# Kernel tuning notes

Measured on AMD Instinct MI355X. Metric: run time of the kernel, lower is better.

## Reference

```python
import jax, jax.numpy as jnp
import numpy as np

NUM_ENT = 40000
NUM_REL = 20


def _rgcn_layer(x, src, dst, et, comp, basis, root, bias, act):
    # Basis decomposition: W_r = sum_b comp[r, b] * basis[b]  -> [R, in, out]
    W = jnp.einsum('rb,bio->rio', comp, basis)
    # Per-(dst, relation) sum of source features: equivalent to per-edge
    # transform W_{et[e]} @ x[src[e]] then scatter-sum, but transforms after
    # aggregation (linear, so identical math) to avoid an [E, in, out] gather.
    seg = dst * NUM_REL + et                       # combined segment id
    S = jax.ops.segment_sum(x[src], seg, num_segments=NUM_ENT * NUM_REL)
    S = S.reshape(NUM_ENT, NUM_REL, x.shape[1])    # [N, R, in]
    agg = jnp.einsum('nri,rio->no', S, W)          # [N, out]
    # mean aggregation over ALL incoming edges (PyG RGCNConv aggr='mean')
    deg = jax.ops.segment_sum(jnp.ones(src.shape[0], x.dtype), dst,
                              num_segments=NUM_ENT)
    agg = agg / jnp.clip(deg, 1.0)[:, None]
    out = agg + x @ root + bias
    return jnp.tanh(out) if act else out


def setup_inputs() -> dict:
    key = jax.random.key(0)
    ks = jax.random.split(key, 16)
    E = 640000
    d = 128
    B = 8
    s = 0.05
    return {
        'edge_index': jax.random.randint(ks[0], (2, E), 0, NUM_ENT),
        'edge_type': jax.random.randint(ks[1], (E,), 0, NUM_REL),
        'init_embed': jax.random.normal(ks[2], (NUM_ENT, d), jnp.float32) * s,
        'init_rel': jax.random.normal(ks[3], (NUM_REL * 2, d), jnp.float32) * s,
        'w_rel': jax.random.normal(ks[4], (d, d), jnp.float32) * s,
        'comp1': jax.random.normal(ks[5], (NUM_REL, B), jnp.float32) * s,
        'basis1': jax.random.normal(ks[6], (B, d, d), jnp.float32) * s,
        'root1': jax.random.normal(ks[7], (d, d), jnp.float32) * s,
        'bias1': jax.random.normal(ks[8], (d,), jnp.float32) * s,
        'comp2': jax.random.normal(ks[9], (NUM_REL, B), jnp.float32) * s,
        'basis2': jax.random.normal(ks[10], (B, d, d), jnp.float32) * s,
        'root2': jax.random.normal(ks[11], (d, d), jnp.float32) * s,
        'bias2': jax.random.normal(ks[12], (d,), jnp.float32) * s,
    }


def reference(edge_index, edge_type, init_embed, init_rel, w_rel,
              comp1, basis1, root1, bias1, comp2, basis2, root2, bias2):
    src, dst = edge_index[0], edge_index[1]
    x = init_embed
    # layer 1: init_dim -> gcn_dim, act=tanh (gcn_layer=2)
    x = _rgcn_layer(x, src, dst, edge_type, comp1, basis1, root1, bias1, True)
    # dropout is identity at inference
    # layer 2: embed_dim -> embed_dim, act=None
    x = _rgcn_layer(x, src, dst, edge_type, comp2, basis2, root2, bias2, False)
    r = init_rel @ w_rel
    return (x, r)
```

## Files before the change

### kernel.cpp

```cpp
#include <hip/hip_runtime.h>
#include <hip/hip_bf16.h>

#define NENT 40000
#define NREL 20
#define DIM 128
#define NBASIS 8
#define TILE 32
#define PKCAP 1024
#define SCANBLK 157

typedef __attribute__((ext_vector_type(8))) short sh8;
typedef __attribute__((ext_vector_type(4))) float fx4;

__device__ __forceinline__ short f2bf(float f) {
    union { __hip_bfloat16 h; short s; } u;
    u.h = __float2bfloat16(f);
    return u.s;
}

__global__ void k_tobf(const float* __restrict__ x, ushort* __restrict__ xb, int nelem) {
    int i = (blockIdx.x * 256 + threadIdx.x) * 4;
    if (i >= nelem) return;
    float4 v = *(const float4*)(x + i);
    ushort4 o;
    o.x = (ushort)f2bf(v.x); o.y = (ushort)f2bf(v.y);
    o.z = (ushort)f2bf(v.z); o.w = (ushort)f2bf(v.w);
    *(ushort4*)(xb + i) = o;
}

__global__ void k_wfrag9(const float* __restrict__ basis, const float* __restrict__ root,
                         short* __restrict__ Wfb) {
    int t = blockIdx.x * 256 + threadIdx.x;
    if (t >= 9 * 16384) return;
    int ks = t / 16384;
    int rem = t & 16383;
    int i = rem >> 7, o = rem & 127;
    float v = (ks < 8) ? basis[ks * 16384 + i * 128 + o] : root[i * 128 + o];
    int c = o >> 4, l15 = o & 15;
    int kk = i >> 5, lhi = (i >> 3) & 3, e = i & 7;
    int lane = l15 + lhi * 16;
    Wfb[(size_t)ks * 16384 + (size_t)(((c * 4 + kk) * 64 + lane) << 3) + e] = f2bf(v);
}

__global__ void k_hist(const int* __restrict__ dst, int E, int* __restrict__ hist) {
    int e = blockIdx.x * 256 + threadIdx.x;
    if (e < E) atomicAdd(&hist[dst[e]], 1);
}

__global__ void k_scan1(const int* __restrict__ hist, int* __restrict__ offs,
                        int* __restrict__ bsum) {
    __shared__ int ps[256];
    int t = threadIdx.x;
    int i = blockIdx.x * 256 + t;
    int v = (i < NENT) ? hist[i] : 0;
    ps[t] = v;
    __syncthreads();
    for (int off = 1; off < 256; off <<= 1) {
        int u = (t >= off) ? ps[t - off] : 0;
        __syncthreads();
        ps[t] += u;
        __syncthreads();
    }
    if (i < NENT) offs[i] = ps[t] - v;
    if (t == 255) bsum[blockIdx.x] = ps[255];
}

__global__ void k_scan2(int* __restrict__ bsum) {
    __shared__ int ps[256];
    int t = threadIdx.x;
    int v = (t < SCANBLK) ? bsum[t] : 0;
    ps[t] = v;
    __syncthreads();
    for (int off = 1; off < 256; off <<= 1) {
        int u = (t >= off) ? ps[t - off] : 0;
        __syncthreads();
        ps[t] += u;
        __syncthreads();
    }
    if (t < SCANBLK) bsum[t] = ps[t] - v;
}

__global__ void k_scan3(int* __restrict__ offs, int* __restrict__ cursor,
                        const int* __restrict__ bsum, int E) {
    int i = blockIdx.x * 256 + threadIdx.x;
    if (i < NENT) {
        int o = offs[i] + bsum[blockIdx.x];
        offs[i] = o;
        cursor[i] = o;
    }
    if (i == 0) offs[NENT] = E;
}

__global__ void k_scatter(const int* __restrict__ et, const int* __restrict__ srcA,
                          const int* __restrict__ dstA, int E,
                          int* __restrict__ cursor, unsigned* __restrict__ packed) {
    int e = blockIdx.x * 256 + threadIdx.x;
    if (e >= E) return;
    int pos = atomicAdd(&cursor[dstA[e]], 1);
    packed[pos] = (unsigned)srcA[e] | ((unsigned)et[e] << 16);
}

#define GLDD(dst, ptr)                                                     \
    asm volatile("global_load_dword %0, %1, off" : "=v"(dst) : "v"(ptr))

#define WAITV(N)                                                           \
    do {                                                                   \
        asm volatile("s_waitcnt vmcnt(" #N ")" ::: "memory");              \
        __builtin_amdgcn_sched_barrier(0);                                 \
    } while (0)

__global__ __launch_bounds__(512) void k_fused(
    const ushort* __restrict__ xb, const unsigned* __restrict__ packed,
    const int* __restrict__ offs, const float* __restrict__ comp,
    const short* __restrict__ Wfb, const float* __restrict__ bias,
    ushort* __restrict__ outbf, float* __restrict__ outf, int act) {
    __shared__ __align__(16) ushort Gl[TILE * 1024];
    __shared__ __align__(16) float cl[NREL * NBASIS];
    __shared__ __align__(16) unsigned pkl[PKCAP];

    int t = threadIdx.x;
    int lane = t & 63, wid = t >> 6;
    if (t < NREL * NBASIS) cl[t] = comp[t];

    int tile0 = blockIdx.x * TILE;
    int base = offs[tile0];
    int totE = offs[tile0 + TILE] - base;
    for (int i = t; i < totE && i < PKCAP; i += 512) pkl[i] = packed[base + i];
    __syncthreads();

    const unsigned* xrow = (const unsigned*)xb + lane;
    bool fast = (totE <= PKCAP);
    for (int sub = 0; sub < 4; ++sub) {
        int row = wid * 4 + sub;
        int n = tile0 + row;
        int begg = offs[n];
        int cnt = offs[n + 1] - begg;
        int begl = begg - base;

        float a0[NBASIS], a1[NBASIS];
#pragma unroll
        for (int b = 0; b < NBASIS; ++b) { a0[b] = 0.f; a1[b] = 0.f; }

        if (cnt > 0 && fast) {
            unsigned p0v = pkl[begl];
            unsigned pA[8], pB[8], rA[8], rB[8];

            auto ldp = [&](int i0, unsigned (&p)[8]) {
#pragma unroll
                for (int u = 0; u < 8; ++u) {
                    int i = i0 + u;
                    p[u] = (i < cnt) ? pkl[begl + i] : p0v;
                }
            };
            auto issue = [&](const unsigned (&p)[8], unsigned (&r)[8]) {
#pragma unroll
                for (int u = 0; u < 8; ++u) {
                    const unsigned* ap = xrow + (size_t)(p[u] & 0xFFFFu) * 64;
                    GLDD(r[u], ap);
                }
            };
            auto proc = [&](int i0, const unsigned (&p)[8], const unsigned (&r)[8]) {
#pragma unroll
                for (int u = 0; u < 8; ++u) {
                    if (i0 + u < cnt) {
                        float xlo = __uint_as_float(r[u] << 16);
                        float xhi = __uint_as_float(r[u] & 0xFFFF0000u);
                        int et = p[u] >> 16;
                        float4 cwa = *(const float4*)&cl[et * NBASIS];
                        float4 cwb = *(const float4*)&cl[et * NBASIS + 4];
                        a0[0] += cwa.x * xlo; a1[0] += cwa.x * xhi;
                        a0[1] += cwa.y * xlo; a1[1] += cwa.y * xhi;
                        a0[2] += cwa.z * xlo; a1[2] += cwa.z * xhi;
                        a0[3] += cwa.w * xlo; a1[3] += cwa.w * xhi;
                        a0[4] += cwb.x * xlo; a1[4] += cwb.x * xhi;
                        a0[5] += cwb.y * xlo; a1[5] += cwb.y * xhi;
                        a0[6] += cwb.z * xlo; a1[6] += cwb.z * xhi;
                        a0[7] += cwb.w * xlo; a1[7] += cwb.w * xhi;
                    }
                }
            };

            ldp(0, pA); issue(pA, rA);
            int i0 = 0;
            while (i0 < cnt) {
                ldp(i0 + 8, pB); issue(pB, rB);
                WAITV(8);
                proc(i0, pA, rA);
                i0 += 8;
                if (i0 >= cnt) break;
                ldp(i0 + 8, pA); issue(pA, rA);
                WAITV(8);
                proc(i0, pB, rB);
                i0 += 8;
            }
            asm volatile("s_waitcnt vmcnt(0)" ::: "memory");
            __builtin_amdgcn_sched_barrier(0);
        } else if (cnt > 0) {
            unsigned pA = packed[begg], pB = 0, rA = xrow[(size_t)(pA & 0xFFFFu) * 64];
            if (cnt > 1) pB = packed[begg + 1];
            for (int i = 0; i < cnt; ++i) {
                unsigned pC = (i + 2 < cnt) ? packed[begg + i + 2] : 0u;
                unsigned rB = xrow[(size_t)(pB & 0xFFFFu) * 64];
                float xlo = __uint_as_float(rA << 16);
                float xhi = __uint_as_float(rA & 0xFFFF0000u);
                int et = pA >> 16;
                float4 cwa = *(const float4*)&cl[et * NBASIS];
                float4 cwb = *(const float4*)&cl[et * NBASIS + 4];
                a0[0] += cwa.x * xlo; a1[0] += cwa.x * xhi;
                a0[1] += cwa.y * xlo; a1[1] += cwa.y * xhi;
                a0[2] += cwa.z * xlo; a1[2] += cwa.z * xhi;
                a0[3] += cwa.w * xlo; a1[3] += cwa.w * xhi;
                a0[4] += cwb.x * xlo; a1[4] += cwb.x * xhi;
                a0[5] += cwb.y * xlo; a1[5] += cwb.y * xhi;
                a0[6] += cwb.z * xlo; a1[6] += cwb.z * xhi;
                a0[7] += cwb.w * xlo; a1[7] += cwb.w * xhi;
                pA = pB; pB = pC; rA = rB;
            }
        }

        float inv = 1.f / (float)(cnt < 1 ? 1 : cnt);
#pragma unroll
        for (int b = 0; b < NBASIS; ++b) {
            unsigned lo = (unsigned)(ushort)f2bf(a0[b] * inv);
            unsigned hi = (unsigned)(ushort)f2bf(a1[b] * inv);
            unsigned byteoff = (unsigned)(row * 2048 + b * 256 + lane * 4);
            byteoff ^= (unsigned)((row & 7) << 4);
            *(unsigned*)((char*)Gl + byteoff) = lo | (hi << 16);
        }
    }
    __syncthreads();

    int wr = wid >> 2, wc = wid & 3;
    int l15 = lane & 15, lhi = lane >> 4;
    int arow = wr * 16 + l15;

    fx4 acc0 = (fx4){0.f, 0.f, 0.f, 0.f};
    fx4 acc1 = (fx4){0.f, 0.f, 0.f, 0.f};

    const ushort* Xr = xb + (size_t)(tile0 + wr * 16 + l15) * 128 + lhi * 8;
    const sh8* W8 = (const sh8*)Wfb;
    int c0 = wc * 2, c1 = wc * 2 + 1;

#pragma unroll
    for (int ks = 0; ks < 9; ++ks) {
        sh8 a[4];
        if (ks < 8) {
#pragma unroll
            for (int kk = 0; kk < 4; ++kk) {
                unsigned byteoff = (unsigned)(arow * 2048 + ks * 256 + kk * 64 + lhi * 16);
                byteoff ^= (unsigned)((arow & 7) << 4);
                a[kk] = *(const sh8*)((const char*)Gl + byteoff);
            }
        } else {
#pragma unroll
            for (int kk = 0; kk < 4; ++kk) a[kk] = *(const sh8*)(Xr + kk * 32);
        }
#pragma unroll
        for (int kk = 0; kk < 4; ++kk) {
            sh8 b0 = W8[(size_t)ks * 2048 + (size_t)((c0 * 4 + kk) * 64 + lane)];
            sh8 b1 = W8[(size_t)ks * 2048 + (size_t)((c1 * 4 + kk) * 64 + lane)];
            acc0 = __builtin_amdgcn_mfma_f32_16x16x32_bf16(a[kk], b0, acc0, 0, 0, 0);
            acc1 = __builtin_amdgcn_mfma_f32_16x16x32_bf16(a[kk], b1, acc1, 0, 0, 0);
        }
    }

    int orow0 = tile0 + wr * 16 + lhi * 4;
#pragma unroll
    for (int cc = 0; cc < 2; ++cc) {
        int col = wc * 32 + cc * 16 + l15;
        float bv = bias[col];
        const fx4& ac = cc ? acc1 : acc0;
#pragma unroll
        for (int j = 0; j < 4; ++j) {
            float v = ac[j] + bv;
            if (act) {
                v = tanhf(v);
                outbf[(size_t)(orow0 + j) * 128 + col] = (ushort)f2bf(v);
            } else {
                outf[(size_t)(orow0 + j) * 128 + col] = v;
            }
        }
    }
}

__global__ void k_rel(const float* __restrict__ rel, const float* __restrict__ wrel,
                      float* __restrict__ out, int nrows) {
    int idx = blockIdx.x * 256 + threadIdx.x;
    if (idx >= nrows * DIM) return;
    int j = idx >> 7, o = idx & 127;
    float s = 0.f;
    for (int i = 0; i < DIM; ++i) s += rel[j * DIM + i] * wrel[i * DIM + o];
    out[idx] = s;
}

extern "C" void kernel_launch(void* const* d_in, const int* in_sizes, int n_in,
                              void* d_out, int out_size, void* d_ws, size_t ws_size,
                              hipStream_t stream) {
    const int* edge_index = (const int*)d_in[0];
    const int* edge_type  = (const int*)d_in[1];
    const float* init_embed = (const float*)d_in[2];
    const float* init_rel   = (const float*)d_in[3];
    const float* w_rel      = (const float*)d_in[4];
    const float* comp1  = (const float*)d_in[5];
    const float* basis1 = (const float*)d_in[6];
    const float* root1  = (const float*)d_in[7];
    const float* bias1  = (const float*)d_in[8];
    const float* comp2  = (const float*)d_in[9];
    const float* basis2 = (const float*)d_in[10];
    const float* root2  = (const float*)d_in[11];
    const float* bias2  = (const float*)d_in[12];

    int E = in_sizes[1];
    const int* src = edge_index;
    const int* dst = edge_index + E;
    int relrows = in_sizes[3] / DIM;

    short* Wfb1 = (short*)d_ws;
    short* Wfb2 = Wfb1 + (size_t)9 * 16384;
    ushort* xb  = (ushort*)(Wfb2 + (size_t)9 * 16384);
    ushort* hb  = xb + (size_t)NENT * DIM;
    int* hist   = (int*)(hb + (size_t)NENT * DIM);
    int* offs   = hist + 40004;
    int* cursor = offs + 40004;
    int* bsum   = cursor + 40004;
    unsigned* packed = (unsigned*)(bsum + 160);

    float* outx = (float*)d_out;
    float* outr = outx + (size_t)NENT * DIM;

    hipMemsetAsync(hist, 0, NENT * sizeof(int), stream);

    k_tobf<<<(NENT * DIM / 4 + 255) / 256, 256, 0, stream>>>(init_embed, xb, NENT * DIM);
    k_wfrag9<<<(9 * 16384 + 255) / 256, 256, 0, stream>>>(basis1, root1, Wfb1);
    k_wfrag9<<<(9 * 16384 + 255) / 256, 256, 0, stream>>>(basis2, root2, Wfb2);
    k_hist<<<(E + 255) / 256, 256, 0, stream>>>(dst, E, hist);
    k_scan1<<<SCANBLK, 256, 0, stream>>>(hist, offs, bsum);
    k_scan2<<<1, 256, 0, stream>>>(bsum);
    k_scan3<<<SCANBLK, 256, 0, stream>>>(offs, cursor, bsum, E);
    k_scatter<<<(E + 255) / 256, 256, 0, stream>>>(edge_type, src, dst, E, cursor, packed);

    k_fused<<<NENT / TILE, 512, 0, stream>>>(xb, packed, offs, comp1, Wfb1, bias1,
                                             hb, outx, 1);
    k_fused<<<NENT / TILE, 512, 0, stream>>>(hb, packed, offs, comp2, Wfb2, bias2,
                                             hb, outx, 0);

    k_rel<<<(relrows * DIM + 255) / 256, 256, 0, stream>>>(init_rel, w_rel, outr, relrows);
}
```

Measured before the change: 241.9 us.

## Use scalar-base gathers, read comp from global, remap MFMA waves to columns

In the gather loop, the edge's source row offset is made wave-uniform with readfirstlane and passed as an SGPR base to global_load_dword, using a per-lane constant offset in place of a 64-bit per-lane address. The LDS copy of the basis coefficients is dropped and they are read straight from global memory, where uniform addresses may become scalar or cached loads. The MFMA stage now gives each of the 8 waves one 16-column block across both 16-row halves, so each wave loads its B fragment once and reuses it twice, at the cost of loading twice as many A fragments.

```diff
diff --git a/kernel.cpp b/kernel.cpp
--- a/kernel.cpp
+++ b/kernel.cpp
@@ -100,8 +100,9 @@
     packed[pos] = (unsigned)srcA[e] | ((unsigned)et[e] << 16);
 }
 
-#define GLDD(dst, ptr)                                                     \
-    asm volatile("global_load_dword %0, %1, off" : "=v"(dst) : "v"(ptr))
+#define GLDS(dst, voff, sbase)                                             \
+    asm volatile("global_load_dword %0, %1, %2"                            \
+                 : "=v"(dst) : "v"(voff), "s"(sbase))
 
 #define WAITV(N)                                                           \
     do {                                                                   \
@@ -115,12 +116,11 @@
     const short* __restrict__ Wfb, const float* __restrict__ bias,
     ushort* __restrict__ outbf, float* __restrict__ outf, int act) {
     __shared__ __align__(16) ushort Gl[TILE * 1024];
-    __shared__ __align__(16) float cl[NREL * NBASIS];
     __shared__ __align__(16) unsigned pkl[PKCAP];
 
     int t = threadIdx.x;
     int lane = t & 63, wid = t >> 6;
-    if (t < NREL * NBASIS) cl[t] = comp[t];
+    unsigned lane4 = (unsigned)(lane * 4);
 
     int tile0 = blockIdx.x * TILE;
     int base = offs[tile0];
@@ -128,7 +128,6 @@
     for (int i = t; i < totE && i < PKCAP; i += 512) pkl[i] = packed[base + i];
     __syncthreads();
 
-    const unsigned* xrow = (const unsigned*)xb + lane;
     bool fast = (totE <= PKCAP);
     for (int sub = 0; sub < 4; ++sub) {
         int row = wid * 4 + sub;
@@ -142,32 +141,35 @@
         for (int b = 0; b < NBASIS; ++b) { a0[b] = 0.f; a1[b] = 0.f; }
 
         if (cnt > 0 && fast) {
-            unsigned p0v = pkl[begl];
-            unsigned pA[8], pB[8], rA[8], rB[8];
-
-            auto ldp = [&](int i0, unsigned (&p)[8]) {
+            int sbA[8], seA[8], sbB[8], seB[8];
+            unsigned rA[8], rB[8];
+
+            auto ldp = [&](int i0, int (&sb)[8], int (&se)[8]) {
 #pragma unroll
                 for (int u = 0; u < 8; ++u) {
                     int i = i0 + u;
-                    p[u] = (i < cnt) ? pkl[begl + i] : p0v;
+                    int li = begl + (i < cnt ? i : 0);
+                    unsigned p = __builtin_amdgcn_readfirstlane(pkl[li]);
+                    sb[u] = (int)(p & 0xFFFFu) * 256;
+                    se[u] = (int)(p >> 16);
                 }
             };
-            auto issue = [&](const unsigned (&p)[8], unsigned (&r)[8]) {
+            auto issue = [&](const int (&sb)[8], unsigned (&r)[8]) {
 #pragma unroll
                 for (int u = 0; u < 8; ++u) {
-                    const unsigned* ap = xrow + (size_t)(p[u] & 0xFFFFu) * 64;
-                    GLDD(r[u], ap);
+                    const char* bp = (const char*)xb + sb[u];
+                    GLDS(r[u], lane4, bp);
                 }
             };
-            auto proc = [&](int i0, const unsigned (&p)[8], const unsigned (&r)[8]) {
+            auto proc = [&](int i0, const int (&se)[8], const unsigned (&r)[8]) {
 #pragma unroll
                 for (int u = 0; u < 8; ++u) {
                     if (i0 + u < cnt) {
+                        const float4* cp = (const float4*)(comp + se[u] * NBASIS);
+                        float4 cwa = cp[0];
+                        float4 cwb = cp[1];
                         float xlo = __uint_as_float(r[u] << 16);
                         float xhi = __uint_as_float(r[u] & 0xFFFF0000u);
-                        int et = p[u] >> 16;
-                        float4 cwa = *(const float4*)&cl[et * NBASIS];
-                        float4 cwb = *(const float4*)&cl[et * NBASIS + 4];
                         a0[0] += cwa.x * xlo; a1[0] += cwa.x * xhi;
                         a0[1] += cwa.y * xlo; a1[1] += cwa.y * xhi;
                         a0[2] += cwa.z * xlo; a1[2] += cwa.z * xhi;
@@ -180,22 +182,23 @@
                 }
             };
 
-            ldp(0, pA); issue(pA, rA);
+            ldp(0, sbA, seA); issue(sbA, rA);
             int i0 = 0;
             while (i0 < cnt) {
-                ldp(i0 + 8, pB); issue(pB, rB);
+                ldp(i0 + 8, sbB, seB); issue(sbB, rB);
                 WAITV(8);
-                proc(i0, pA, rA);
+                proc(i0, seA, rA);
                 i0 += 8;
                 if (i0 >= cnt) break;
-                ldp(i0 + 8, pA); issue(pA, rA);
+                ldp(i0 + 8, sbA, seA); issue(sbA, rA);
                 WAITV(8);
-                proc(i0, pB, rB);
+                proc(i0, seB, rB);
                 i0 += 8;
             }
             asm volatile("s_waitcnt vmcnt(0)" ::: "memory");
             __builtin_amdgcn_sched_barrier(0);
         } else if (cnt > 0) {
+            const unsigned* xrow = (const unsigned*)xb + lane;
             unsigned pA = packed[begg], pB = 0, rA = xrow[(size_t)(pA & 0xFFFFu) * 64];
             if (cnt > 1) pB = packed[begg + 1];
             for (int i = 0; i < cnt; ++i) {
@@ -204,8 +207,9 @@
                 float xlo = __uint_as_float(rA << 16);
                 float xhi = __uint_as_float(rA & 0xFFFF0000u);
                 int et = pA >> 16;
-                float4 cwa = *(const float4*)&cl[et * NBASIS];
-                float4 cwb = *(const float4*)&cl[et * NBASIS + 4];
+                const float4* cp = (const float4*)(comp + et * NBASIS);
+                float4 cwa = cp[0];
+                float4 cwb = cp[1];
                 a0[0] += cwa.x * xlo; a1[0] += cwa.x * xhi;
                 a0[1] += cwa.y * xlo; a1[1] += cwa.y * xhi;
                 a0[2] += cwa.z * xlo; a1[2] += cwa.z * xhi;
@@ -230,46 +234,49 @@
     }
     __syncthreads();
 
-    int wr = wid >> 2, wc = wid & 3;
     int l15 = lane & 15, lhi = lane >> 4;
-    int arow = wr * 16 + l15;
+    int c = wid;
 
     fx4 acc0 = (fx4){0.f, 0.f, 0.f, 0.f};
     fx4 acc1 = (fx4){0.f, 0.f, 0.f, 0.f};
 
-    const ushort* Xr = xb + (size_t)(tile0 + wr * 16 + l15) * 128 + lhi * 8;
     const sh8* W8 = (const sh8*)Wfb;
-    int c0 = wc * 2, c1 = wc * 2 + 1;
 
 #pragma unroll
     for (int ks = 0; ks < 9; ++ks) {
-        sh8 a[4];
+        sh8 a0f[4], a1f[4];
         if (ks < 8) {
 #pragma unroll
             for (int kk = 0; kk < 4; ++kk) {
-                unsigned byteoff = (unsigned)(arow * 2048 + ks * 256 + kk * 64 + lhi * 16);
-                byteoff ^= (unsigned)((arow & 7) << 4);
-                a[kk] = *(const sh8*)((const char*)Gl + byteoff);
+                int ar0 = l15, ar1 = 16 + l15;
+                unsigned bo0 = (unsigned)(ar0 * 2048 + ks * 256 + kk * 64 + lhi * 16);
+                unsigned bo1 = (unsigned)(ar1 * 2048 + ks * 256 + kk * 64 + lhi * 16);
+                bo0 ^= (unsigned)((ar0 & 7) << 4);
+                bo1 ^= (unsigned)((ar1 & 7) << 4);
+                a0f[kk] = *(const sh8*)((const char*)Gl + bo0);
+                a1f[kk] = *(const sh8*)((const char*)Gl + bo1);
             }
         } else {
 #pragma unroll
-            for (int kk = 0; kk < 4; ++kk) a[kk] = *(const sh8*)(Xr + kk * 32);
+            for (int kk = 0; kk < 4; ++kk) {
+                a0f[kk] = *(const sh8*)(xb + (size_t)(tile0 + l15) * 128 + lhi * 8 + kk * 32);
+                a1f[kk] = *(const sh8*)(xb + (size_t)(tile0 + 16 + l15) * 128 + lhi * 8 + kk * 32);
+            }
         }
 #pragma unroll
         for (int kk = 0; kk < 4; ++kk) {
-            sh8 b0 = W8[(size_t)ks * 2048 + (size_t)((c0 * 4 + kk) * 64 + lane)];
-            sh8 b1 = W8[(size_t)ks * 2048 + (size_t)((c1 * 4 + kk) * 64 + lane)];
-            acc0 = __builtin_amdgcn_mfma_f32_16x16x32_bf16(a[kk], b0, acc0, 0, 0, 0);
-            acc1 = __builtin_amdgcn_mfma_f32_16x16x32_bf16(a[kk], b1, acc1, 0, 0, 0);
-        }
-    }
-
-    int orow0 = tile0 + wr * 16 + lhi * 4;
-#pragma unroll
-    for (int cc = 0; cc < 2; ++cc) {
-        int col = wc * 32 + cc * 16 + l15;
-        float bv = bias[col];
-        const fx4& ac = cc ? acc1 : acc0;
+            sh8 b = W8[(size_t)ks * 2048 + (size_t)((c * 4 + kk) * 64 + lane)];
+            acc0 = __builtin_amdgcn_mfma_f32_16x16x32_bf16(a0f[kk], b, acc0, 0, 0, 0);
+            acc1 = __builtin_amdgcn_mfma_f32_16x16x32_bf16(a1f[kk], b, acc1, 0, 0, 0);
+        }
+    }
+
+    int col = c * 16 + l15;
+    float bv = bias[col];
+#pragma unroll
+    for (int rg = 0; rg < 2; ++rg) {
+        const fx4& ac = rg ? acc1 : acc0;
+        int orow0 = tile0 + rg * 16 + lhi * 4;
 #pragma unroll
         for (int j = 0; j < 4; ++j) {
             float v = ac[j] + bv;
```

Result: faster. 229.7 us (-5.1%).
